# Kernel optimization log

Hardware: AMD Instinct MI355X
Metric: run time of the kernel (lower is better)

The kernel has to match this reference:

```python
import jax, jax.numpy as jnp
import numpy as np

DIM = 512
HEADS = 8
DIM_HEAD = 64
HIDDEN = HEADS * DIM_HEAD  # 512
B, C, H, W = 32, DIM, 32, 32


def setup_inputs() -> dict:
    key = jax.random.key(0)
    ks = jax.random.split(key, 7)
    s_in = 1.0 / np.sqrt(DIM)
    s_h = 1.0 / np.sqrt(HIDDEN)
    x = jax.random.normal(ks[0], (B, C, H, W), dtype=jnp.float32)
    Wq = jax.random.uniform(ks[1], (DIM, HIDDEN), jnp.float32, -s_in, s_in)
    Wk = jax.random.uniform(ks[2], (DIM, HIDDEN), jnp.float32, -s_in, s_in)
    Wv = jax.random.uniform(ks[3], (DIM, HIDDEN), jnp.float32, -s_in, s_in)
    Wp = jax.random.uniform(ks[4], (HIDDEN, DIM), jnp.float32, -s_h, s_h)
    bp = jax.random.uniform(ks[5], (DIM,), jnp.float32, -s_h, s_h)
    return {"x": x, "Wq": Wq, "Wk": Wk, "Wv": Wv, "Wp": Wp, "bp": bp}


def reference(x, Wq, Wk, Wv, Wp, bp):
    b, c, h, w = x.shape
    n = h * w
    xt = x.reshape(b, c, n).transpose(0, 2, 1)  # [B, N, C]
    q = (xt @ Wq).reshape(b, n, HEADS, DIM_HEAD)
    k = (xt @ Wk).reshape(b, n, HEADS, DIM_HEAD)
    v = (xt @ Wv).reshape(b, n, HEADS, DIM_HEAD)
    k_softmax = jax.nn.softmax(k, axis=1)  # softmax over tokens N
    context = jnp.einsum('bnhd,bnhv->bhdv', k_softmax, v)  # [B, H, D, D]
    out = jnp.einsum('bnhd,bhdv->bnhv', q, context).reshape(b, n, HIDDEN)
    out = out @ Wp + bp  # [B, N, C]
    return out.transpose(0, 2, 1).reshape(b, c, h, w)
```

## Files before the change

kernel.cpp:

```cpp
#include <hip/hip_runtime.h>
#include <hip/hip_bf16.h>


__device__ __forceinline__ float bf2f(unsigned short u) {
    union { unsigned int i; float f; } x;
    x.i = ((unsigned int)u) << 16;
    return x.f;
}
__device__ __forceinline__ unsigned short f2bf(float f) {
    unsigned int u = __float_as_uint(f);
    unsigned int lsb = (u >> 16) & 1u;
    u += 0x7fffu + lsb;
    return (unsigned short)(u >> 16);
}
__device__ __forceinline__ float waveReduceMax(float v) {
    #pragma unroll
    for (int off = 32; off > 0; off >>= 1) v = fmaxf(v, __shfl_xor(v, off, 64));
    return v;
}
__device__ __forceinline__ float waveReduceSum(float v) {
    #pragma unroll
    for (int off = 32; off > 0; off >>= 1) v += __shfl_xor(v, off, 64);
    return v;
}

typedef __bf16 bf16x8 __attribute__((ext_vector_type(8)));
typedef float  f32x4  __attribute__((ext_vector_type(4)));

__global__ void detect_dtype(const unsigned short* __restrict__ x, int* __restrict__ flag)
{
    int t = threadIdx.x;
    unsigned short u = x[2 * t];
    int e = (u >> 7) & 0xFF;
    int sane = (e >= 113 && e <= 142) ? 1 : 0;
    #pragma unroll
    for (int off = 32; off > 0; off >>= 1) sane += __shfl_xor(sane, off, 64);
    if (t == 0) *flag = (sane >= 32) ? 1 : 0;
}

__global__ __launch_bounds__(256) void transpose_x(
    const void* __restrict__ in, unsigned short* __restrict__ out,
    const int* __restrict__ flag)
{
    const int fl = *flag;
    const int b  = blockIdx.z;
    const int c0 = blockIdx.x * 64;
    const int r0 = blockIdx.y * 64;
    __shared__ unsigned short Ts[64][68];
    const int t   = threadIdx.x;
    const int tr  = t >> 4;
    const int tc4 = (t & 15) * 4;
    #pragma unroll
    for (int rr = 0; rr < 4; ++rr) {
        int rl = rr * 16 + tr;
        long off = (long)b * 524288 + (long)(r0 + rl) * 1024 + c0 + tc4;
        unsigned short v[4];
        if (fl) {
            ushort4 u = *(const ushort4*)((const unsigned short*)in + off);
            v[0] = u.x; v[1] = u.y; v[2] = u.z; v[3] = u.w;
        } else {
            float4 u = *(const float4*)((const float*)in + off);
            v[0] = f2bf(u.x); v[1] = f2bf(u.y); v[2] = f2bf(u.z); v[3] = f2bf(u.w);
        }
        #pragma unroll
        for (int q = 0; q < 4; ++q) Ts[tc4 + q][rl] = v[q];
    }
    __syncthreads();
    #pragma unroll
    for (int rr = 0; rr < 4; ++rr) {
        int cl = rr * 16 + tr;
        ushort4 o = *(const ushort4*)&Ts[cl][tc4];
        *(ushort4*)(out + (long)b * 524288 + (long)(c0 + cl) * 512 + r0 + tc4) = o;
    }
}

__global__ __launch_bounds__(256) void transpose_w3(
    const void* __restrict__ w0, const void* __restrict__ w1,
    const void* __restrict__ w2, unsigned short* __restrict__ out,
    const int* __restrict__ flag)
{
    const int fl = *flag;
    const int z  = blockIdx.z;
    const void* in = (z == 0) ? w0 : (z == 1) ? w1 : w2;
    unsigned short* op = out + (long)z * 262144;
    const int c0 = blockIdx.x * 64;
    const int r0 = blockIdx.y * 64;
    __shared__ unsigned short Ts[64][68];
    const int t   = threadIdx.x;
    const int tr  = t >> 4;
    const int tc4 = (t & 15) * 4;
    #pragma unroll
    for (int rr = 0; rr < 4; ++rr) {
        int rl = rr * 16 + tr;
        long off = (long)(r0 + rl) * 512 + c0 + tc4;
        unsigned short v[4];
        if (fl) {
            ushort4 u = *(const ushort4*)((const unsigned short*)in + off);
            v[0] = u.x; v[1] = u.y; v[2] = u.z; v[3] = u.w;
        } else {
            float4 u = *(const float4*)((const float*)in + off);
            v[0] = f2bf(u.x); v[1] = f2bf(u.y); v[2] = f2bf(u.z); v[3] = f2bf(u.w);
        }
        #pragma unroll
        for (int q = 0; q < 4; ++q) Ts[tc4 + q][rl] = v[q];
    }
    __syncthreads();
    #pragma unroll
    for (int rr = 0; rr < 4; ++rr) {
        int cl = rr * 16 + tr;
        ushort4 o = *(const ushort4*)&Ts[cl][tc4];
        *(ushort4*)(op + (long)(c0 + cl) * 512 + r0 + tc4) = o;
    }
}

__global__ __launch_bounds__(256) void gemm_bt_mfma(
    const unsigned short* __restrict__ A, long a_bstride,
    const unsigned short* __restrict__ Bm, long b_bstride,
    void* __restrict__ C, long c_bstride,
    const void* __restrict__ bias,
    int M, int N, int K, int mode,
    const int* __restrict__ flag)
{
    const int b  = blockIdx.z;
    const int n0 = blockIdx.x * 128;
    const int m0 = blockIdx.y * 128;
    const unsigned short* Ab = A  + (long)b * a_bstride;
    const unsigned short* Bb = Bm + (long)b * b_bstride;

    __shared__ unsigned short As[128 * 40];
    __shared__ unsigned short Bs[128 * 40];

    const int t    = threadIdx.x;
    const int w    = t >> 6;
    const int lane = t & 63;
    const int wm   = (w & 1) * 64;
    const int wn   = (w >> 1) * 64;
    const int fm   = lane & 15;
    const int kg   = lane >> 4;

    const int srow = t >> 2;
    const int scol = (t & 3) * 8;

    f32x4 acc[4][4] = {};

    uint4 a0 = *(const uint4*)(Ab + (long)(m0 + srow)      * K + scol);
    uint4 a1 = *(const uint4*)(Ab + (long)(m0 + srow + 64) * K + scol);
    uint4 b0 = *(const uint4*)(Bb + (long)(n0 + srow)      * K + scol);
    uint4 b1 = *(const uint4*)(Bb + (long)(n0 + srow + 64) * K + scol);

    for (int k0 = 0; k0 < K; k0 += 32) {
        __syncthreads();
        *(uint4*)&As[srow * 40 + scol]        = a0;
        *(uint4*)&As[(srow + 64) * 40 + scol] = a1;
        *(uint4*)&Bs[srow * 40 + scol]        = b0;
        *(uint4*)&Bs[(srow + 64) * 40 + scol] = b1;
        __syncthreads();

        if (k0 + 32 < K) {
            const int kn = k0 + 32;
            a0 = *(const uint4*)(Ab + (long)(m0 + srow)      * K + kn + scol);
            a1 = *(const uint4*)(Ab + (long)(m0 + srow + 64) * K + kn + scol);
            b0 = *(const uint4*)(Bb + (long)(n0 + srow)      * K + kn + scol);
            b1 = *(const uint4*)(Bb + (long)(n0 + srow + 64) * K + kn + scol);
        }

        bf16x8 af[4], bf[4];
        #pragma unroll
        for (int i = 0; i < 4; ++i)
            af[i] = *(const bf16x8*)&As[(wm + i * 16 + fm) * 40 + kg * 8];
        #pragma unroll
        for (int j = 0; j < 4; ++j)
            bf[j] = *(const bf16x8*)&Bs[(wn + j * 16 + fm) * 40 + kg * 8];
        #pragma unroll
        for (int i = 0; i < 4; ++i)
            #pragma unroll
            for (int j = 0; j < 4; ++j)
                acc[i][j] = __builtin_amdgcn_mfma_f32_16x16x32_bf16(
                    af[i], bf[j], acc[i][j], 0, 0, 0);
    }

    const int fl = *flag;
    const long cb = (long)b * c_bstride;
    #pragma unroll
    for (int i = 0; i < 4; ++i) {
        #pragma unroll
        for (int j = 0; j < 4; ++j) {
            const int n = n0 + wn + j * 16 + fm;
            #pragma unroll
            for (int r = 0; r < 4; ++r) {
                const int m = m0 + wm + i * 16 + kg * 4 + r;
                const float val = acc[i][j][r];
                if (mode == 0) {
                    ((unsigned short*)C)[cb + (long)m * N + n] = f2bf(val);
                } else {
                    float bv = 0.f;
                    if (bias) bv = fl ? bf2f(((const unsigned short*)bias)[m])
                                      : ((const float*)bias)[m];
                    const long off = cb + (long)m * N + n;
                    if (fl) ((unsigned short*)C)[off] = f2bf(val + bv);
                    else    ((float*)C)[off] = val + bv;
                }
            }
        }
    }
}

__global__ __launch_bounds__(256) void softmax_rows(unsigned short* __restrict__ KV)
{
    const long row = blockIdx.x;
    unsigned short* p = KV + ((row >> 9) << 20) + ((row & 511) << 10);
    const int t = threadIdx.x;

    ushort4 raw = *(const ushort4*)(p + t * 4);
    float f[4] = {bf2f(raw.x), bf2f(raw.y), bf2f(raw.z), bf2f(raw.w)};

    float m = fmaxf(fmaxf(f[0], f[1]), fmaxf(f[2], f[3]));
    m = waveReduceMax(m);
    __shared__ float redm[4], reds[4];
    if ((t & 63) == 0) redm[t >> 6] = m;
    __syncthreads();
    m = fmaxf(fmaxf(redm[0], redm[1]), fmaxf(redm[2], redm[3]));

    float e[4], s = 0.f;
    #pragma unroll
    for (int i = 0; i < 4; ++i) { e[i] = expf(f[i] - m); s += e[i]; }
    s = waveReduceSum(s);
    if ((t & 63) == 0) reds[t >> 6] = s;
    __syncthreads();
    s = reds[0] + reds[1] + reds[2] + reds[3];
    const float inv = 1.0f / s;

    ushort4 o;
    o.x = f2bf(e[0] * inv); o.y = f2bf(e[1] * inv);
    o.z = f2bf(e[2] * inv); o.w = f2bf(e[3] * inv);
    *(ushort4*)(p + t * 4) = o;
}

__global__ __launch_bounds__(256) void ctx_mfma(
    const unsigned short* __restrict__ KV, float* __restrict__ ctx)
{
    const int bh = blockIdx.x;
    const unsigned short* Kb = KV + ((long)(bh >> 3) << 20) + (long)(bh & 7) * 65536;
    const unsigned short* Vb = Kb + 524288;

    const int t    = threadIdx.x;
    const int w    = t >> 6;
    const int lane = t & 63;
    const int fm   = lane & 15;
    const int kg   = lane >> 4;

    f32x4 acc[4][4] = {};

    #pragma unroll 2
    for (int c = 0; c < 8; ++c) {
        const int k0 = w * 256 + c * 32;
        bf16x8 af[4], bf[4];
        #pragma unroll
        for (int i = 0; i < 4; ++i)
            af[i] = *(const bf16x8*)(Kb + (long)(i * 16 + fm) * 1024 + k0 + kg * 8);
        #pragma unroll
        for (int j = 0; j < 4; ++j)
            bf[j] = *(const bf16x8*)(Vb + (long)(j * 16 + fm) * 1024 + k0 + kg * 8);
        #pragma unroll
        for (int i = 0; i < 4; ++i)
            #pragma unroll
            for (int j = 0; j < 4; ++j)
                acc[i][j] = __builtin_amdgcn_mfma_f32_16x16x32_bf16(
                    af[i], bf[j], acc[i][j], 0, 0, 0);
    }

    __shared__ float red[64][65];
    for (int ph = 0; ph < 4; ++ph) {
        if (w == ph) {
            #pragma unroll
            for (int i = 0; i < 4; ++i)
                #pragma unroll
                for (int j = 0; j < 4; ++j)
                    #pragma unroll
                    for (int r = 0; r < 4; ++r) {
                        const int m = i * 16 + kg * 4 + r;
                        const int n = j * 16 + fm;
                        if (ph == 0) red[m][n]  = acc[i][j][r];
                        else         red[m][n] += acc[i][j][r];
                    }
        }
        __syncthreads();
    }
    float* cp = ctx + (long)bh * 4096;
    for (int i = t; i < 4096; i += 256) cp[i] = red[i >> 6][i & 63];
}

__global__ __launch_bounds__(256) void weff_kernel(
    const float* __restrict__ ctx,
    const void* __restrict__ Wp,
    unsigned short* __restrict__ WeffT,
    const int* __restrict__ flag)
{
    const int fl = *flag;
    const int c0 = blockIdx.x * 64;
    const int h  = blockIdx.y;
    const int b  = blockIdx.z;

    __shared__ float Cs[64][65];
    __shared__ float Ws[64][68];

    const int t = threadIdx.x;
    const int tx = t & 15, ty = t >> 4;

    const float* cb = ctx + ((long)b * 8 + h) * 4096;
    for (int i = t; i < 4096; i += 256) Cs[i >> 6][i & 63] = cb[i];
    for (int i = t; i < 4096; i += 256) {
        int v = i >> 6, c = i & 63;
        long idx = (long)(h * 64 + v) * 512 + c0 + c;
        Ws[v][c] = fl ? bf2f(((const unsigned short*)Wp)[idx])
                      : ((const float*)Wp)[idx];
    }
    __syncthreads();

    float acc[4][4];
    #pragma unroll
    for (int i = 0; i < 4; ++i)
        #pragma unroll
        for (int j = 0; j < 4; ++j) acc[i][j] = 0.f;

    #pragma unroll
    for (int v = 0; v < 64; ++v) {
        float a[4], d[4];
        #pragma unroll
        for (int i = 0; i < 4; ++i) a[i] = Ws[v][ty * 4 + i];
        #pragma unroll
        for (int j = 0; j < 4; ++j) d[j] = Cs[tx * 4 + j][v];
        #pragma unroll
        for (int i = 0; i < 4; ++i)
            #pragma unroll
            for (int j = 0; j < 4; ++j) acc[i][j] += a[i] * d[j];
    }
    #pragma unroll
    for (int i = 0; i < 4; ++i) {
        ushort4 o;
        o.x = f2bf(acc[i][0]); o.y = f2bf(acc[i][1]);
        o.z = f2bf(acc[i][2]); o.w = f2bf(acc[i][3]);
        *(ushort4*)&WeffT[((long)b * 512 + c0 + ty * 4 + i) * 512 + h * 64 + tx * 4] = o;
    }
}

extern "C" void kernel_launch(void* const* d_in, const int* in_sizes, int n_in,
                              void* d_out, int out_size, void* d_ws, size_t ws_size,
                              hipStream_t stream) {
    const void* x  = d_in[0];
    const void* Wq = d_in[1];
    const void* Wk = d_in[2];
    const void* Wv = d_in[3];
    const void* Wp = d_in[4];
    const void* bp = d_in[5];

    char* ws = (char*)d_ws;
    unsigned short* Xt    = (unsigned short*)(ws);
    unsigned short* KV    = (unsigned short*)(ws + 33554432ll);
    unsigned short* Q     = (unsigned short*)(ws + 33554432ll);
    float*          ctx   = (float*)(ws + 100663296ll);
    unsigned short* WeffT = (unsigned short*)(ws + 104857600ll);
    unsigned short* WT    = (unsigned short*)(ws + 121634816ll);
    int*            flag  = (int*)(ws + 123207680ll);

    detect_dtype<<<dim3(1), dim3(64), 0, stream>>>((const unsigned short*)x, flag);

    transpose_x<<<dim3(16, 8, 32), 256, 0, stream>>>(x, Xt, flag);
    transpose_w3<<<dim3(8, 8, 3), 256, 0, stream>>>(Wq, Wk, Wv, WT, flag);

    const long XB = 1024ll * 512;
    gemm_bt_mfma<<<dim3(8, 8, 32), 256, 0, stream>>>(
        WT + 262144, 0, Xt, XB, KV, 1048576ll, nullptr, 1024, 1024, 512, 0, flag);

    softmax_rows<<<dim3(16384), 256, 0, stream>>>(KV);
    ctx_mfma<<<dim3(256), 256, 0, stream>>>(KV, ctx);
    weff_kernel<<<dim3(8, 8, 32), 256, 0, stream>>>(ctx, Wp, WeffT, flag);

    gemm_bt_mfma<<<dim3(4, 8, 32), 256, 0, stream>>>(
        Xt, XB, WT, 0, Q, XB, nullptr, 1024, 512, 512, 0, flag);

    gemm_bt_mfma<<<dim3(8, 4, 32), 256, 0, stream>>>(
        WeffT, 262144ll, Q, XB, d_out, 524288ll, bp, 512, 1024, 512, 2, flag);
}
```

Baseline: 337.3 us.

## Fold Wq into per-batch projection weights and split context reduction across blocks

Drops the per-token Q projection GEMM (32×1024×512×512). Instead, Wq is multiplied into the per-batch effective projection weight, a 512×512×512 GEMM per batch, and the fused weight is applied directly to the transposed input. The context kernel is split across 4 token slices so it launches four times as many blocks, and the weff kernel sums the partials when it loads them. The GEMM shared-memory row pitch also changes from 40 to 32 elements, which removes padding but may add LDS bank conflicts.

```diff
diff --git a/kernel.cpp b/kernel.cpp
--- a/kernel.cpp
+++ b/kernel.cpp
@@ -74,14 +74,13 @@
     }
 }
 
-__global__ __launch_bounds__(256) void transpose_w3(
+__global__ __launch_bounds__(256) void transpose_w2(
     const void* __restrict__ w0, const void* __restrict__ w1,
-    const void* __restrict__ w2, unsigned short* __restrict__ out,
-    const int* __restrict__ flag)
+    unsigned short* __restrict__ out, const int* __restrict__ flag)
 {
     const int fl = *flag;
     const int z  = blockIdx.z;
-    const void* in = (z == 0) ? w0 : (z == 1) ? w1 : w2;
+    const void* in = (z == 0) ? w0 : w1;
     unsigned short* op = out + (long)z * 262144;
     const int c0 = blockIdx.x * 64;
     const int r0 = blockIdx.y * 64;
@@ -113,6 +112,22 @@
     }
 }
 
+__global__ __launch_bounds__(256) void cast_wq(
+    const void* __restrict__ in, unsigned short* __restrict__ out,
+    const int* __restrict__ flag)
+{
+    const int fl = *flag;
+    const long idx = ((long)blockIdx.x * 256 + threadIdx.x) * 4;
+    if (fl) {
+        *(ushort4*)(out + idx) = *(const ushort4*)((const unsigned short*)in + idx);
+    } else {
+        float4 u = *(const float4*)((const float*)in + idx);
+        ushort4 o;
+        o.x = f2bf(u.x); o.y = f2bf(u.y); o.z = f2bf(u.z); o.w = f2bf(u.w);
+        *(ushort4*)(out + idx) = o;
+    }
+}
+
 __global__ __launch_bounds__(256) void gemm_bt_mfma(
     const unsigned short* __restrict__ A, long a_bstride,
     const unsigned short* __restrict__ Bm, long b_bstride,
@@ -127,8 +142,8 @@
     const unsigned short* Ab = A  + (long)b * a_bstride;
     const unsigned short* Bb = Bm + (long)b * b_bstride;
 
-    __shared__ unsigned short As[128 * 40];
-    __shared__ unsigned short Bs[128 * 40];
+    __shared__ unsigned short As[128 * 32];
+    __shared__ unsigned short Bs[128 * 32];
 
     const int t    = threadIdx.x;
     const int w    = t >> 6;
@@ -150,10 +165,10 @@
 
     for (int k0 = 0; k0 < K; k0 += 32) {
         __syncthreads();
-        *(uint4*)&As[srow * 40 + scol]        = a0;
-        *(uint4*)&As[(srow + 64) * 40 + scol] = a1;
-        *(uint4*)&Bs[srow * 40 + scol]        = b0;
-        *(uint4*)&Bs[(srow + 64) * 40 + scol] = b1;
+        *(uint4*)&As[srow * 32 + scol]        = a0;
+        *(uint4*)&As[(srow + 64) * 32 + scol] = a1;
+        *(uint4*)&Bs[srow * 32 + scol]        = b0;
+        *(uint4*)&Bs[(srow + 64) * 32 + scol] = b1;
         __syncthreads();
 
         if (k0 + 32 < K) {
@@ -167,10 +182,10 @@
         bf16x8 af[4], bf[4];
         #pragma unroll
         for (int i = 0; i < 4; ++i)
-            af[i] = *(const bf16x8*)&As[(wm + i * 16 + fm) * 40 + kg * 8];
+            af[i] = *(const bf16x8*)&As[(wm + i * 16 + fm) * 32 + kg * 8];
         #pragma unroll
         for (int j = 0; j < 4; ++j)
-            bf[j] = *(const bf16x8*)&Bs[(wn + j * 16 + fm) * 40 + kg * 8];
+            bf[j] = *(const bf16x8*)&Bs[(wn + j * 16 + fm) * 32 + kg * 8];
         #pragma unroll
         for (int i = 0; i < 4; ++i)
             #pragma unroll
@@ -237,9 +252,10 @@
 }
 
 __global__ __launch_bounds__(256) void ctx_mfma(
-    const unsigned short* __restrict__ KV, float* __restrict__ ctx)
+    const unsigned short* __restrict__ KV, float* __restrict__ ctxp)
 {
     const int bh = blockIdx.x;
+    const int s  = blockIdx.y;
     const unsigned short* Kb = KV + ((long)(bh >> 3) << 20) + (long)(bh & 7) * 65536;
     const unsigned short* Vb = Kb + 524288;
 
@@ -251,9 +267,9 @@
 
     f32x4 acc[4][4] = {};
 
-    #pragma unroll 2
-    for (int c = 0; c < 8; ++c) {
-        const int k0 = w * 256 + c * 32;
+    #pragma unroll
+    for (int c = 0; c < 2; ++c) {
+        const int k0 = s * 256 + w * 64 + c * 32;
         bf16x8 af[4], bf[4];
         #pragma unroll
         for (int i = 0; i < 4; ++i)
@@ -286,12 +302,12 @@
         }
         __syncthreads();
     }
-    float* cp = ctx + (long)bh * 4096;
+    float* cp = ctxp + (long)s * 1048576 + (long)bh * 4096;
     for (int i = t; i < 4096; i += 256) cp[i] = red[i >> 6][i & 63];
 }
 
 __global__ __launch_bounds__(256) void weff_kernel(
-    const float* __restrict__ ctx,
+    const float* __restrict__ ctxp,
     const void* __restrict__ Wp,
     unsigned short* __restrict__ WeffT,
     const int* __restrict__ flag)
@@ -307,8 +323,9 @@
     const int t = threadIdx.x;
     const int tx = t & 15, ty = t >> 4;
 
-    const float* cb = ctx + ((long)b * 8 + h) * 4096;
-    for (int i = t; i < 4096; i += 256) Cs[i >> 6][i & 63] = cb[i];
+    const float* cb = ctxp + ((long)b * 8 + h) * 4096;
+    for (int i = t; i < 4096; i += 256)
+        Cs[i >> 6][i & 63] = cb[i] + cb[i + 1048576] + cb[i + 2097152] + cb[i + 3145728];
     for (int i = t; i < 4096; i += 256) {
         int v = i >> 6, c = i & 63;
         long idx = (long)(h * 64 + v) * 512 + c0 + c;
@@ -357,28 +374,30 @@
     char* ws = (char*)d_ws;
     unsigned short* Xt    = (unsigned short*)(ws);
     unsigned short* KV    = (unsigned short*)(ws + 33554432ll);
-    unsigned short* Q     = (unsigned short*)(ws + 33554432ll);
-    float*          ctx   = (float*)(ws + 100663296ll);
-    unsigned short* WeffT = (unsigned short*)(ws + 104857600ll);
-    unsigned short* WT    = (unsigned short*)(ws + 121634816ll);
-    int*            flag  = (int*)(ws + 123207680ll);
+    unsigned short* WeffT = (unsigned short*)(ws + 33554432ll);
+    unsigned short* Wfold = (unsigned short*)(ws + 50331648ll);
+    float*          ctxp  = (float*)(ws + 100663296ll);
+    unsigned short* WT    = (unsigned short*)(ws + 117440512ll);
+    unsigned short* Wqb   = (unsigned short*)(ws + 118489088ll);
+    int*            flag  = (int*)(ws + 119013376ll);
 
     detect_dtype<<<dim3(1), dim3(64), 0, stream>>>((const unsigned short*)x, flag);
 
     transpose_x<<<dim3(16, 8, 32), 256, 0, stream>>>(x, Xt, flag);
-    transpose_w3<<<dim3(8, 8, 3), 256, 0, stream>>>(Wq, Wk, Wv, WT, flag);
+    transpose_w2<<<dim3(8, 8, 2), 256, 0, stream>>>(Wk, Wv, WT, flag);
+    cast_wq<<<dim3(256), 256, 0, stream>>>(Wq, Wqb, flag);
 
     const long XB = 1024ll * 512;
     gemm_bt_mfma<<<dim3(8, 8, 32), 256, 0, stream>>>(
-        WT + 262144, 0, Xt, XB, KV, 1048576ll, nullptr, 1024, 1024, 512, 0, flag);
+        WT, 0, Xt, XB, KV, 1048576ll, nullptr, 1024, 1024, 512, 0, flag);
 
     softmax_rows<<<dim3(16384), 256, 0, stream>>>(KV);
-    ctx_mfma<<<dim3(256), 256, 0, stream>>>(KV, ctx);
-    weff_kernel<<<dim3(8, 8, 32), 256, 0, stream>>>(ctx, Wp, WeffT, flag);
-
-    gemm_bt_mfma<<<dim3(4, 8, 32), 256, 0, stream>>>(
-        Xt, XB, WT, 0, Q, XB, nullptr, 1024, 512, 512, 0, flag);
+    ctx_mfma<<<dim3(256, 4), 256, 0, stream>>>(KV, ctxp);
+    weff_kernel<<<dim3(8, 8, 32), 256, 0, stream>>>(ctxp, Wp, WeffT, flag);
+
+    gemm_bt_mfma<<<dim3(4, 4, 32), 256, 0, stream>>>(
+        WeffT, 262144ll, Wqb, 0, Wfold, 262144ll, nullptr, 512, 512, 512, 0, flag);
 
     gemm_bt_mfma<<<dim3(8, 4, 32), 256, 0, stream>>>(
-        WeffT, 262144ll, Q, XB, d_out, 524288ll, bp, 512, 1024, 512, 2, flag);
-}
+        Wfold, 262144ll, Xt, XB, d_out, 524288ll, bp, 512, 1024, 512, 2, flag);
+}
```

Measured after the change: 344.0 us. No clear change (+2.0%).
